# Kernel tuning notes

Hardware: AMD Instinct MI355X
Metric: run time of the kernel (lower is better)

## Reference

```python
import jax, jax.numpy as jnp
import numpy as np

NUM_HEADS = 4   # num_heads init kwarg
KERNEL = 7      # kernel_size init kwarg
EPS = 1e-5      # nn.LayerNorm default eps


def setup_inputs() -> dict:
    key = jax.random.key(0)
    ks = jax.random.split(key, 6)
    C, depth = 128, 2
    x = jax.random.normal(ks[0], (2, C, 64, 64), jnp.float32)
    qkv_w = jax.random.normal(ks[1], (depth, 3 * C, C), jnp.float32) * 0.05
    qkv_b = jnp.zeros((depth, 3 * C), jnp.float32)
    rpb = jax.random.normal(ks[2], (depth, NUM_HEADS, 2 * KERNEL - 1, 2 * KERNEL - 1), jnp.float32) * 0.02
    proj_w = jax.random.normal(ks[3], (depth, C, C), jnp.float32) * 0.05
    proj_b = jnp.zeros((depth, C), jnp.float32)
    ln_g = jnp.ones((C,), jnp.float32)
    ln_b = jnp.zeros((C,), jnp.float32)
    return dict(x=x, qkv_w=qkv_w, qkv_b=qkv_b, rpb=rpb,
                proj_w=proj_w, proj_b=proj_b, ln_g=ln_g, ln_b=ln_b)


def _na2d(x, w_qkv, b_qkv, rpb, w_p, b_p):
    """NATTEN-style 2D neighborhood attention. x: (B,H,W,C)."""
    B, H, W, C = x.shape
    h, k = NUM_HEADS, KERNEL
    d = C // h
    qkv = (x @ w_qkv.T + b_qkv).reshape(B, H, W, 3, h, d)
    q = qkv[..., 0, :, :] * (d ** -0.5)   # (B,H,W,h,d)
    kk = qkv[..., 1, :, :]
    v = qkv[..., 2, :, :]
    # edge-clamped window starts: each query sees exactly k x k neighbors
    si = jnp.clip(jnp.arange(H) - k // 2, 0, H - k)
    sj = jnp.clip(jnp.arange(W) - k // 2, 0, W - k)
    idx_i = si[:, None] + jnp.arange(k)   # (H,k) absolute row indices
    idx_j = sj[:, None] + jnp.arange(k)   # (W,k) absolute col indices

    def win(t):  # (B,H,W,h,d) -> (B,H,W,k,k,h,d)
        t = t[:, idx_i]          # (B,H,k,W,h,d)
        t = t[:, :, :, idx_j]    # (B,H,k,W,k,h,d)
        return jnp.transpose(t, (0, 1, 3, 2, 4, 5, 6))

    kw = win(kk)
    vw = win(v)
    attn = jnp.einsum('bijhd,bijpqhd->bijhpq', q, kw)  # (B,H,W,h,k,k)
    # relative position bias: index = (neighbor_abs - query) + (k-1)
    bi = jnp.arange(k)[None, :] + (k - 1) - (jnp.arange(H) - si)[:, None]  # (H,k)
    bj = jnp.arange(k)[None, :] + (k - 1) - (jnp.arange(W) - sj)[:, None]  # (W,k)
    bias = rpb[:, bi[:, None, :, None], bj[None, :, None, :]]  # (h,H,W,k,k)
    attn = attn + jnp.transpose(bias, (1, 2, 0, 3, 4))[None]
    attn = jax.nn.softmax(attn.reshape(B, H, W, h, k * k), axis=-1).reshape(B, H, W, h, k, k)
    out = jnp.einsum('bijhpq,bijpqhd->bijhd', attn, vw).reshape(B, H, W, C)
    return out @ w_p.T + b_p


def reference(x, qkv_w, qkv_b, rpb, proj_w, proj_b, ln_g, ln_b):
    y = jnp.transpose(x, (0, 2, 3, 1))  # NCHW -> NHWC
    for l in range(qkv_w.shape[0]):     # depth=2 stacked NA layers
        y = _na2d(y, qkv_w[l], qkv_b[l], rpb[l], proj_w[l], proj_b[l])
    mu = y.mean(-1, keepdims=True)
    var = y.var(-1, keepdims=True)
    y = (y - mu) / jnp.sqrt(var + EPS) * ln_g + ln_b
    return jnp.transpose(y, (0, 3, 1, 2))  # NHWC -> NCHW
```

## Files before the change

kernel.cpp:

```cpp
#include <hip/hip_runtime.h>
#include <hip/hip_bf16.h>
#include <math.h>

#define PIX 8192
typedef __hip_bfloat16 bf16;
typedef __attribute__((ext_vector_type(8))) short short8;
typedef __attribute__((ext_vector_type(4))) float f32x4;

__device__ inline float bflo(unsigned u) { return __uint_as_float(u << 16); }
__device__ inline float bfhi(unsigned u) { return __uint_as_float(u & 0xffff0000u); }
__device__ inline unsigned short f2b(float f) {
  __hip_bfloat16 h = __float2bfloat16(f);
  return *reinterpret_cast<unsigned short*>(&h);
}
__device__ inline unsigned pack2(float a, float b) {
  return (unsigned)f2b(a) | ((unsigned)f2b(b) << 16);
}
__device__ inline short8 ldw8(const float* __restrict__ p) {
  f32x4 lo = *(const f32x4*)p;
  f32x4 hi = *(const f32x4*)(p + 4);
  short8 r;
  r[0] = (short)f2b(lo[0]); r[1] = (short)f2b(lo[1]);
  r[2] = (short)f2b(lo[2]); r[3] = (short)f2b(lo[3]);
  r[4] = (short)f2b(hi[0]); r[5] = (short)f2b(hi[1]);
  r[6] = (short)f2b(hi[2]); r[7] = (short)f2b(hi[3]);
  return r;
}

__global__ __launch_bounds__(256) void xqkv_cvt(const float* __restrict__ x,
                                                const float* __restrict__ qw,
                                                const float* __restrict__ qb,
                                                unsigned short* __restrict__ qkv,
                                                const float* __restrict__ pw,
                                                unsigned short* __restrict__ wq1,
                                                unsigned short* __restrict__ wp) {
  if (blockIdx.x >= 512) {
    int idx = (blockIdx.x - 512) * 256 + threadIdx.x;
    wq1[idx] = f2b(qw[49152 + idx]);
    wq1[idx + 16384] = f2b(qw[49152 + idx + 16384]);
    if (idx < 16384) wq1[idx + 32768] = f2b(qw[49152 + idx + 32768]);
    wp[idx] = f2b(pw[idx]);
    return;
  }

  __shared__ __align__(16) unsigned short As[16 * 136];
  int m0 = blockIdx.x * 16;
  int tid = threadIdx.x;
  int b = m0 >> 12, i = (m0 >> 6) & 63, j0 = m0 & 63;

  for (int idx = tid; idx < 2048; idx += 256) {
    int c = idx >> 4, jl = idx & 15;
    As[jl * 136 + c] =
        f2b(x[(size_t)b * 524288 + (size_t)c * 4096 + i * 64 + j0 + jl]);
  }
  __syncthreads();

  int w = tid >> 6, lane = tid & 63;
  int quad = lane >> 4, l16 = lane & 15;
  short8 a[4];
#pragma unroll
  for (int kc = 0; kc < 4; ++kc)
    a[kc] = *(const short8*)(As + l16 * 136 + kc * 32 + quad * 8);
#pragma unroll
  for (int nt = 0; nt < 6; ++nt) {
    int col = w * 96 + nt * 16 + l16;
    const float* wrow = qw + (size_t)col * 128 + quad * 8;
    f32x4 c = {0.f, 0.f, 0.f, 0.f};
#pragma unroll
    for (int kc = 0; kc < 4; ++kc)
      c = __builtin_amdgcn_mfma_f32_16x16x32_bf16(a[kc], ldw8(wrow + kc * 32), c, 0, 0, 0);
    float bv = qb[col];
#pragma unroll
    for (int r2 = 0; r2 < 4; ++r2)
      qkv[(size_t)(m0 + quad * 4 + r2) * 384 + col] = f2b(c[r2] + bv);
  }
}

#define RSTRIDE 136
template <int MODE>
__global__ __launch_bounds__(256, 2) void attnproj(const unsigned short* __restrict__ qkvp,
                                                   const float* __restrict__ rpb,
                                                   const unsigned short* __restrict__ wp,
                                                   const float* __restrict__ pbias,
                                                   const unsigned short* __restrict__ wq1,
                                                   const float* __restrict__ qb1,
                                                   unsigned short* __restrict__ qkvo,
                                                   const float* __restrict__ g,
                                                   const float* __restrict__ bta,
                                                   float* __restrict__ out) {
  __shared__ __align__(16) unsigned short kbuf[100 * RSTRIDE];
  __shared__ __align__(16) unsigned short vbuf[100 * RSTRIDE];
  __shared__ float rb[676];

  int ti = blockIdx.x >> 4, tj = blockIdx.x & 15;
  int bz = blockIdx.y;
  int tid = threadIdx.x;
  int bi0 = ti * 4 - 3, bj0 = tj * 4 - 3;

  int r = tid & 3;
  int hh = (tid >> 2) & 3;
  int px = tid >> 4;
  int pi = px >> 2, pj = px & 3;
  int i = ti * 4 + pi, j = tj * 4 + pj;
  int pix = (bz * 64 + i) * 64 + j;
  uint4 qt = *(const uint4*)(qkvp + (size_t)pix * 384 + hh * 32 + r * 8);

  const float LOG2E = 1.44269504088896341f;
  for (int t = tid; t < 676; t += 256) rb[t] = rpb[t] * LOG2E;

  for (int t = tid; t < 3200; t += 256) {
    int row = t >> 5;
    int sub = t & 31;
    int isv = sub >> 4;
    int c = sub & 15;
    int ri = row / 10, rj = row - ri * 10;
    int gi = bi0 + ri, gj = bj0 + rj;
    uint4 val = make_uint4(0, 0, 0, 0);
    if ((unsigned)gi < 64u && (unsigned)gj < 64u) {
      int pixn = (bz * 64 + gi) * 64 + gj;
      val = *(const uint4*)(qkvp + (size_t)pixn * 384 + 128 + isv * 128 + c * 8);
    }
    *(uint4*)((isv ? vbuf : kbuf) + row * RSTRIDE + c * 8) = val;
  }
  __syncthreads();

  int si = min(max(i - 3, 0), 57), sj = min(max(j - 3, 0), 57);
  int li = si - bi0, lj = sj - bj0;
  int oi = i - si, oj = j - sj;

  const float scale = 0.17677669529663687f * 1.44269504088896341f;
  float q[8];
  q[0] = bflo(qt.x) * scale;  q[1] = bfhi(qt.x) * scale;
  q[2] = bflo(qt.y) * scale;  q[3] = bfhi(qt.y) * scale;
  q[4] = bflo(qt.z) * scale;  q[5] = bfhi(qt.z) * scale;
  q[6] = bflo(qt.w) * scale;  q[7] = bfhi(qt.w) * scale;

  const unsigned short* kh = kbuf + hh * 32 + r * 8;
  const unsigned short* vh = vbuf + hh * 32 + r * 8;
  const float* rbh = rb + hh * 169;

  float sum = 0.f;
  float acc[8] = {0.f, 0.f, 0.f, 0.f, 0.f, 0.f, 0.f, 0.f};
#pragma unroll 1
  for (int pp = 0; pp < 7; ++pp) {
#pragma unroll
    for (int qq = 0; qq < 7; ++qq) {
      int nn = (li + pp) * 10 + (lj + qq);
      uint4 tk = *(const uint4*)(kh + nn * RSTRIDE);
      float dot = q[0] * bflo(tk.x) + q[1] * bfhi(tk.x)
                + q[2] * bflo(tk.y) + q[3] * bfhi(tk.y)
                + q[4] * bflo(tk.z) + q[5] * bfhi(tk.z)
                + q[6] * bflo(tk.w) + q[7] * bfhi(tk.w);
      dot += __shfl_xor(dot, 1);
      dot += __shfl_xor(dot, 2);
      float e = __builtin_amdgcn_exp2f(dot + rbh[(pp + 6 - oi) * 13 + (qq + 6 - oj)]);
      sum += e;
      uint4 tv = *(const uint4*)(vh + nn * RSTRIDE);
      acc[0] += e * bflo(tv.x);  acc[1] += e * bfhi(tv.x);
      acc[2] += e * bflo(tv.y);  acc[3] += e * bfhi(tv.y);
      acc[4] += e * bflo(tv.z);  acc[5] += e * bfhi(tv.z);
      acc[6] += e * bflo(tv.w);  acc[7] += e * bfhi(tv.w);
    }
  }
  float inv = 1.f / sum;
  uint4 t;
  t.x = pack2(acc[0] * inv, acc[1] * inv);
  t.y = pack2(acc[2] * inv, acc[3] * inv);
  t.z = pack2(acc[4] * inv, acc[5] * inv);
  t.w = pack2(acc[6] * inv, acc[7] * inv);
  __syncthreads();
  unsigned short* obuf = kbuf;
  *(uint4*)(obuf + px * RSTRIDE + hh * 32 + r * 8) = t;
  __syncthreads();

  unsigned short* ybuf = vbuf;
  int w = tid >> 6, lane = tid & 63;
  int quad = lane >> 4, l16 = lane & 15;
  {
    short8 a[4];
#pragma unroll
    for (int kc = 0; kc < 4; ++kc)
      a[kc] = *(const short8*)(obuf + l16 * RSTRIDE + kc * 32 + quad * 8);
#pragma unroll
    for (int s = 0; s < 2; ++s) {
      int col = w * 32 + s * 16 + l16;
      const short8* bp = (const short8*)(wp + (size_t)col * 128 + quad * 8);
      f32x4 c = {0.f, 0.f, 0.f, 0.f};
#pragma unroll
      for (int kc = 0; kc < 4; ++kc)
        c = __builtin_amdgcn_mfma_f32_16x16x32_bf16(a[kc], bp[kc * 4], c, 0, 0, 0);
      float bv = pbias[col];
#pragma unroll
      for (int r2 = 0; r2 < 4; ++r2)
        ybuf[(quad * 4 + r2) * RSTRIDE + col] = f2b(c[r2] + bv);
    }
  }
  __syncthreads();

  if constexpr (MODE == 0) {
    short8 ay[4];
#pragma unroll
    for (int kc = 0; kc < 4; ++kc)
      ay[kc] = *(const short8*)(ybuf + l16 * RSTRIDE + kc * 32 + quad * 8);
#pragma unroll
    for (int s = 0; s < 6; ++s) {
      int col = (w * 6 + s) * 16 + l16;
      const short8* bp = (const short8*)(wq1 + (size_t)col * 128 + quad * 8);
      float bv = qb1[col];
      f32x4 c = {0.f, 0.f, 0.f, 0.f};
#pragma unroll
      for (int kc = 0; kc < 4; ++kc)
        c = __builtin_amdgcn_mfma_f32_16x16x32_bf16(ay[kc], bp[kc * 4], c, 0, 0, 0);
#pragma unroll
      for (int r2 = 0; r2 < 4; ++r2) {
        int mloc = quad * 4 + r2;
        int gpix = (bz * 64 + ti * 4 + (mloc >> 2)) * 64 + tj * 4 + (mloc & 3);
        qkvo[(size_t)gpix * 384 + col] = f2b(c[r2] + bv);
      }
    }
  } else {
    int px2 = tid >> 4, sub = tid & 15;
    uint4 tv = *(const uint4*)(ybuf + px2 * RSTRIDE + sub * 8);
    float v[8];
    v[0] = bflo(tv.x); v[1] = bfhi(tv.x); v[2] = bflo(tv.y); v[3] = bfhi(tv.y);
    v[4] = bflo(tv.z); v[5] = bfhi(tv.z); v[6] = bflo(tv.w); v[7] = bfhi(tv.w);
    float sum2 = 0.f, sumsq = 0.f;
#pragma unroll
    for (int k = 0; k < 8; ++k) { sum2 += v[k]; sumsq += v[k] * v[k]; }
    sum2 += __shfl_xor(sum2, 1);  sumsq += __shfl_xor(sumsq, 1);
    sum2 += __shfl_xor(sum2, 2);  sumsq += __shfl_xor(sumsq, 2);
    sum2 += __shfl_xor(sum2, 4);  sumsq += __shfl_xor(sumsq, 4);
    sum2 += __shfl_xor(sum2, 8);  sumsq += __shfl_xor(sumsq, 8);
    float mu = sum2 * (1.f / 128.f);
    float rstd = rsqrtf(sumsq * (1.f / 128.f) - mu * mu + 1e-5f);
    int i2 = ti * 4 + (px2 >> 2), j2 = tj * 4 + (px2 & 3);
    int c0 = sub * 8;
    f32x4 g0 = *(const f32x4*)(g + c0),   g1 = *(const f32x4*)(g + c0 + 4);
    f32x4 b0 = *(const f32x4*)(bta + c0), b1 = *(const f32x4*)(bta + c0 + 4);
#pragma unroll
    for (int k = 0; k < 8; ++k) {
      float gg = (k < 4) ? g0[k] : g1[k - 4];
      float bb = (k < 4) ? b0[k] : b1[k - 4];
      float o = (v[k] - mu) * rstd * gg + bb;
      out[(((size_t)bz * 128 + c0 + k) * 64 + i2) * 64 + j2] = o;
    }
  }
}

extern "C" void kernel_launch(void* const* d_in, const int* in_sizes, int n_in,
                              void* d_out, int out_size, void* d_ws, size_t ws_size,
                              hipStream_t stream) {
  (void)in_sizes; (void)n_in; (void)out_size; (void)ws_size;
  const float* x   = (const float*)d_in[0];
  const float* qw  = (const float*)d_in[1];
  const float* qb  = (const float*)d_in[2];
  const float* rpb = (const float*)d_in[3];
  const float* pw  = (const float*)d_in[4];
  const float* pb  = (const float*)d_in[5];
  const float* lg  = (const float*)d_in[6];
  const float* lb  = (const float*)d_in[7];

  unsigned short* qkvA = (unsigned short*)d_ws;
  unsigned short* qkvB = qkvA + (size_t)PIX * 384;
  unsigned short* wq1  = qkvB + (size_t)PIX * 384;
  unsigned short* wp   = wq1 + 49152;
  float* out = (float*)d_out;

  xqkv_cvt<<<640, 256, 0, stream>>>(x, qw, qb, qkvA, pw, wq1, wp);
  attnproj<0><<<dim3(256, 2), 256, 0, stream>>>(qkvA, rpb, wp, pb, wq1,
                                                qb + 384, qkvB, nullptr,
                                                nullptr, nullptr);
  attnproj<1><<<dim3(256, 2), 256, 0, stream>>>(qkvB, rpb + 676, wp + 16384,
                                                pb + 128, nullptr, nullptr,
                                                nullptr, lg, lb, out);
}
```

Measured before the change: 122.9 us.

## Split first QKV projection into transpose-convert kernel and separate bf16 MFMA GEMM

Replaces the fused kernel, which converted x and ran the layer-0 QKV GEMM reading fp32 weights per block, with two kernels. The first transposes and converts x to bf16 NHWC and converts all weights to bf16. The second is a tiled 64x64 MFMA GEMM that reads bf16 operands. The aim is to stop every block re-reading and re-converting fp32 weights and to vectorise the transpose loads. The cost is an extra kernel launch and a round trip of the bf16 activations through global memory.

New measurement: 122.3 us. About the same (-0.5%).

```diff
diff --git a/kernel.cpp b/kernel.cpp
--- a/kernel.cpp
+++ b/kernel.cpp
@@ -16,63 +16,79 @@
 __device__ inline unsigned pack2(float a, float b) {
   return (unsigned)f2b(a) | ((unsigned)f2b(b) << 16);
 }
-__device__ inline short8 ldw8(const float* __restrict__ p) {
-  f32x4 lo = *(const f32x4*)p;
-  f32x4 hi = *(const f32x4*)(p + 4);
-  short8 r;
-  r[0] = (short)f2b(lo[0]); r[1] = (short)f2b(lo[1]);
-  r[2] = (short)f2b(lo[2]); r[3] = (short)f2b(lo[3]);
-  r[4] = (short)f2b(hi[0]); r[5] = (short)f2b(hi[1]);
-  r[6] = (short)f2b(hi[2]); r[7] = (short)f2b(hi[3]);
-  return r;
-}
-
-__global__ __launch_bounds__(256) void xqkv_cvt(const float* __restrict__ x,
-                                                const float* __restrict__ qw,
-                                                const float* __restrict__ qb,
-                                                unsigned short* __restrict__ qkv,
-                                                const float* __restrict__ pw,
-                                                unsigned short* __restrict__ wq1,
-                                                unsigned short* __restrict__ wp) {
+
+__global__ __launch_bounds__(256) void cvt_trans(const float* __restrict__ x,
+                                                 const float* __restrict__ qw,
+                                                 const float* __restrict__ pw,
+                                                 unsigned short* __restrict__ xT,
+                                                 unsigned short* __restrict__ wq,
+                                                 unsigned short* __restrict__ wp) {
   if (blockIdx.x >= 512) {
     int idx = (blockIdx.x - 512) * 256 + threadIdx.x;
-    wq1[idx] = f2b(qw[49152 + idx]);
-    wq1[idx + 16384] = f2b(qw[49152 + idx + 16384]);
-    if (idx < 16384) wq1[idx + 32768] = f2b(qw[49152 + idx + 32768]);
+    wq[idx] = f2b(qw[idx]);
+    wq[idx + 32768] = f2b(qw[idx + 32768]);
+    wq[idx + 65536] = f2b(qw[idx + 65536]);
     wp[idx] = f2b(pw[idx]);
     return;
   }
 
-  __shared__ __align__(16) unsigned short As[16 * 136];
+  __shared__ __align__(16) unsigned short T[16][136];
   int m0 = blockIdx.x * 16;
   int tid = threadIdx.x;
   int b = m0 >> 12, i = (m0 >> 6) & 63, j0 = m0 & 63;
 
-  for (int idx = tid; idx < 2048; idx += 256) {
-    int c = idx >> 4, jl = idx & 15;
-    As[jl * 136 + c] =
-        f2b(x[(size_t)b * 524288 + (size_t)c * 4096 + i * 64 + j0 + jl]);
-  }
-  __syncthreads();
-
+  int c = tid >> 1, half = tid & 1;
+  const float* src = x + (size_t)b * 524288 + (size_t)c * 4096 + i * 64 + j0 + half * 8;
+  f32x4 v0 = *(const f32x4*)src;
+  f32x4 v1 = *(const f32x4*)(src + 4);
+#pragma unroll
+  for (int k = 0; k < 4; ++k) T[half * 8 + k][c] = f2b(v0[k]);
+#pragma unroll
+  for (int k = 0; k < 4; ++k) T[half * 8 + 4 + k][c] = f2b(v1[k]);
+  __syncthreads();
+
+  int px = tid >> 4, u = tid & 15;
+  uint4 o = *(const uint4*)(&T[px][u * 8]);
+  *(uint4*)(xT + (size_t)(m0 + px) * 128 + u * 8) = o;
+}
+
+__global__ __launch_bounds__(256) void gemm_mfma(const unsigned short* __restrict__ A,
+                                                 const unsigned short* __restrict__ W,
+                                                 const float* __restrict__ bias,
+                                                 unsigned short* __restrict__ Cmat,
+                                                 int N) {
+  int m0 = blockIdx.x * 64, n0 = blockIdx.y * 64;
+  int tid = threadIdx.x;
   int w = tid >> 6, lane = tid & 63;
   int quad = lane >> 4, l16 = lane & 15;
+
+  const short8* ap =
+      (const short8*)(A + (size_t)(m0 + w * 16 + l16) * 128 + quad * 8);
   short8 a[4];
 #pragma unroll
-  for (int kc = 0; kc < 4; ++kc)
-    a[kc] = *(const short8*)(As + l16 * 136 + kc * 32 + quad * 8);
-#pragma unroll
-  for (int nt = 0; nt < 6; ++nt) {
-    int col = w * 96 + nt * 16 + l16;
-    const float* wrow = qw + (size_t)col * 128 + quad * 8;
+  for (int kc = 0; kc < 4; ++kc) a[kc] = ap[kc * 4];
+
+  f32x4 acc[4];
+#pragma unroll
+  for (int nt = 0; nt < 4; ++nt) {
+    const short8* bp =
+        (const short8*)(W + (size_t)(n0 + nt * 16 + l16) * 128 + quad * 8);
     f32x4 c = {0.f, 0.f, 0.f, 0.f};
 #pragma unroll
     for (int kc = 0; kc < 4; ++kc)
-      c = __builtin_amdgcn_mfma_f32_16x16x32_bf16(a[kc], ldw8(wrow + kc * 32), c, 0, 0, 0);
-    float bv = qb[col];
-#pragma unroll
-    for (int r2 = 0; r2 < 4; ++r2)
-      qkv[(size_t)(m0 + quad * 4 + r2) * 384 + col] = f2b(c[r2] + bv);
+      c = __builtin_amdgcn_mfma_f32_16x16x32_bf16(a[kc], bp[kc * 4], c, 0, 0, 0);
+    acc[nt] = c;
+  }
+
+#pragma unroll
+  for (int nt = 0; nt < 4; ++nt) {
+    int col = n0 + nt * 16 + l16;
+    float bv = bias[col];
+#pragma unroll
+    for (int r = 0; r < 4; ++r) {
+      int m = m0 + w * 16 + quad * 4 + r;
+      Cmat[(size_t)m * N + col] = f2b(acc[nt][r] + bv);
+    }
   }
 }
 
@@ -260,16 +276,18 @@
   const float* lg  = (const float*)d_in[6];
   const float* lb  = (const float*)d_in[7];
 
-  unsigned short* qkvA = (unsigned short*)d_ws;
+  unsigned short* xT   = (unsigned short*)d_ws;
+  unsigned short* qkvA = xT + (size_t)PIX * 128;
   unsigned short* qkvB = qkvA + (size_t)PIX * 384;
-  unsigned short* wq1  = qkvB + (size_t)PIX * 384;
-  unsigned short* wp   = wq1 + 49152;
+  unsigned short* wq   = qkvB + (size_t)PIX * 384;
+  unsigned short* wp   = wq + 98304;
   float* out = (float*)d_out;
 
-  xqkv_cvt<<<640, 256, 0, stream>>>(x, qw, qb, qkvA, pw, wq1, wp);
-  attnproj<0><<<dim3(256, 2), 256, 0, stream>>>(qkvA, rpb, wp, pb, wq1,
-                                                qb + 384, qkvB, nullptr,
-                                                nullptr, nullptr);
+  cvt_trans<<<640, 256, 0, stream>>>(x, qw, pw, xT, wq, wp);
+  gemm_mfma<<<dim3(128, 6), 256, 0, stream>>>(xT, wq, qb, qkvA, 384);
+  attnproj<0><<<dim3(256, 2), 256, 0, stream>>>(qkvA, rpb, wp, pb,
+                                                wq + 49152, qb + 384, qkvB,
+                                                nullptr, nullptr, nullptr);
   attnproj<1><<<dim3(256, 2), 256, 0, stream>>>(qkvB, rpb + 676, wp + 16384,
                                                 pb + 128, nullptr, nullptr,
                                                 nullptr, lg, lb, out);
```
